# Performance work log

Measured on AMD Instinct MI355X. Metric: run time of the kernel, lower is better.

The kernel has to match this reference:

```python
import jax, jax.numpy as jnp
import numpy as np

INPUT_DIM = 3
OUTPUT_DIM = 3
HIDDEN = 128


def _lstm_layer(x, W_ih, W_hh, b_ih, b_hh):
    # x: (B, T, D_in); W_ih: (4H, D_in); W_hh: (4H, H); biases: (4H,)
    B, T, _ = x.shape
    H = W_hh.shape[1]
    # precompute input contribution for all timesteps (one big GEMM)
    xg = jnp.einsum('bti,gi->btg', x, W_ih) + b_ih + b_hh  # (B, T, 4H)
    h0 = jnp.zeros((B, H), dtype=x.dtype)
    c0 = jnp.zeros((B, H), dtype=x.dtype)

    def step(carry, xt):
        h, c = carry
        g = xt + h @ W_hh.T  # (B, 4H)
        i, f, gg, o = jnp.split(g, 4, axis=-1)  # PyTorch gate order: i, f, g, o
        i = jax.nn.sigmoid(i)
        f = jax.nn.sigmoid(f)
        gg = jnp.tanh(gg)
        o = jax.nn.sigmoid(o)
        c = f * c + i * gg
        h = o * jnp.tanh(c)
        return (h, c), h

    _, hs = jax.lax.scan(step, (h0, c0), jnp.swapaxes(xg, 0, 1))  # hs: (T, B, H)
    return jnp.swapaxes(hs, 0, 1)  # (B, T, H)


def setup_inputs() -> dict:
    key = jax.random.key(0)
    ks = jax.random.split(key, 11)
    B, T = 256, 1000
    s_in = 1.0 / np.sqrt(HIDDEN)
    inp = {
        'x': jax.random.normal(ks[0], (B, T, INPUT_DIM), dtype=jnp.float32),
        'W_ih_l0': jax.random.uniform(ks[1], (4 * HIDDEN, INPUT_DIM), jnp.float32, -s_in, s_in),
        'W_hh_l0': jax.random.uniform(ks[2], (4 * HIDDEN, HIDDEN), jnp.float32, -s_in, s_in),
        'b_ih_l0': jax.random.uniform(ks[3], (4 * HIDDEN,), jnp.float32, -s_in, s_in),
        'b_hh_l0': jax.random.uniform(ks[4], (4 * HIDDEN,), jnp.float32, -s_in, s_in),
        'W_ih_l1': jax.random.uniform(ks[5], (4 * HIDDEN, HIDDEN), jnp.float32, -s_in, s_in),
        'W_hh_l1': jax.random.uniform(ks[6], (4 * HIDDEN, HIDDEN), jnp.float32, -s_in, s_in),
        'b_ih_l1': jax.random.uniform(ks[7], (4 * HIDDEN,), jnp.float32, -s_in, s_in),
        'b_hh_l1': jax.random.uniform(ks[8], (4 * HIDDEN,), jnp.float32, -s_in, s_in),
        'fc_w': jax.random.uniform(ks[9], (OUTPUT_DIM, HIDDEN), jnp.float32, -s_in, s_in),
        'fc_b': jax.random.uniform(ks[10], (OUTPUT_DIM,), jnp.float32, -s_in, s_in),
    }
    return inp


def reference(x, W_ih_l0, W_hh_l0, b_ih_l0, b_hh_l0,
              W_ih_l1, W_hh_l1, b_ih_l1, b_hh_l1, fc_w, fc_b):
    # 2-layer LSTM (eval mode: inter-layer dropout is identity) + linear head
    h1 = _lstm_layer(x, W_ih_l0, W_hh_l0, b_ih_l0, b_hh_l0)
    h2 = _lstm_layer(h1, W_ih_l1, W_hh_l1, b_ih_l1, b_hh_l1)
    y = jnp.einsum('bth,oh->bto', h2, fc_w) + fc_b  # (B, T, OUTPUT_DIM)
    return y
```

## Files before the change

kernel.cpp:

```cpp
#include <hip/hip_runtime.h>

#define NB 256
#define TT 1000
#define HD 128
#define NG 512

#define WGA __attribute__((amdgpu_flat_work_group_size(512,512), amdgpu_waves_per_eu(2,2)))

typedef __attribute__((ext_vector_type(8))) short s8v;
typedef __attribute__((ext_vector_type(4))) float f4v;

__device__ __forceinline__ unsigned short bf16rne(float v) {
    unsigned u = __float_as_uint(v);
    unsigned r = u + 0x7FFF + ((u >> 16) & 1);
    return (unsigned short)(r >> 16);
}
__device__ __forceinline__ float bf16tof(unsigned short h) {
    return __uint_as_float(((unsigned)h) << 16);
}
__device__ __forceinline__ float sigf(float x) { return 1.f / (1.f + __expf(-x)); }
__device__ __forceinline__ float tanhfast(float x) {
    float e = __expf(-2.f * x);
    return 2.f / (1.f + e) - 1.f;
}

#define PKFMA(acc, h, w) \
    asm("v_pk_fma_f32 %0, %1, %2, %0" : "+v"(acc) : "v"(h), "v"(w))

__device__ __forceinline__ float2 lo2(float4 v) { return make_float2(v.x, v.y); }
__device__ __forceinline__ float2 hi2(float4 v) { return make_float2(v.z, v.w); }

#define DOT128P(h4, wv, P0, P1, P2, P3)                                        \
    {                                                                          \
        _Pragma("unroll")                                                      \
        for (int g = 0; g < 8; ++g) {                                          \
            float4 c0=(h4)[4*g+0], c1=(h4)[4*g+1],                             \
                   c2=(h4)[4*g+2], c3=(h4)[4*g+3];                             \
            PKFMA(P0, lo2(c0), lo2(wv[4*g+0]));                                \
            PKFMA(P1, hi2(c0), hi2(wv[4*g+0]));                                \
            PKFMA(P2, lo2(c1), lo2(wv[4*g+1]));                                \
            PKFMA(P3, hi2(c1), hi2(wv[4*g+1]));                                \
            PKFMA(P0, lo2(c2), lo2(wv[4*g+2]));                                \
            PKFMA(P1, hi2(c2), hi2(wv[4*g+2]));                                \
            PKFMA(P2, lo2(c3), lo2(wv[4*g+3]));                                \
            PKFMA(P3, hi2(c3), hi2(wv[4*g+3]));                                \
            __builtin_amdgcn_sched_barrier(0);                                 \
        }                                                                      \
    }

__global__ WGA
void lstm_layer0(const float* __restrict__ x,
                 const float* __restrict__ Wih, const float* __restrict__ Whh,
                 const float* __restrict__ bih, const float* __restrict__ bhh,
                 float* __restrict__ h1c,
                 float* __restrict__ hstate, float* __restrict__ cstate,
                 int t0, int len)
{
    __shared__ __align__(16) float h_lds[HD];
    __shared__ float gbuf[NG];
    __shared__ float x_lds[3 * TT];
    const int j = threadIdx.x;
    const int b = blockIdx.x;

    float4 wv[HD/4];
    {
        const float4* wr = (const float4*)(Whh + (size_t)j * HD);
        #pragma unroll
        for (int q = 0; q < HD/4; ++q) wv[q] = wr[q];
    }
    const float wx0 = Wih[j*3+0], wx1 = Wih[j*3+1], wx2 = Wih[j*3+2];
    const float bias = bih[j] + bhh[j];

    for (int idx = j; idx < 3*len; idx += 512)
        x_lds[idx] = x[((size_t)b*TT + t0)*3 + idx];

    float c = 0.f, hcur = 0.f;
    if (j < HD) {
        if (t0 != 0) { hcur = hstate[b*HD+j]; c = cstate[b*HD+j]; }
        h_lds[j] = hcur;
    }
    __syncthreads();

    const int gtype = j >> 7;
    for (int tc = 0; tc < len; ++tc) {
        float2 p0 = {0.f,0.f}, p1 = {0.f,0.f}, p2 = {0.f,0.f}, p3 = {0.f,0.f};
        const float4* h4 = (const float4*)h_lds;
        DOT128P(h4, wv, p0, p1, p2, p3);
        float acc = bias + ((p0.x+p0.y)+(p1.x+p1.y)) + ((p2.x+p2.y)+(p3.x+p3.y));
        acc = fmaf(wx0, x_lds[3*tc+0], acc);
        acc = fmaf(wx1, x_lds[3*tc+1], acc);
        acc = fmaf(wx2, x_lds[3*tc+2], acc);
        float act = (gtype == 2) ? tanhfast(acc) : sigf(acc);
        gbuf[j] = act;
        __syncthreads();
        if (j < HD) {
            float ig = gbuf[j], fg = gbuf[HD+j], gg = gbuf[2*HD+j], og = gbuf[3*HD+j];
            c = fmaf(fg, c, ig*gg);
            hcur = og * tanhfast(c);
            h_lds[j] = hcur;
            h1c[((size_t)b*len + tc)*HD + j] = hcur;
        }
        __syncthreads();
    }
    if (j < HD) { hstate[b*HD+j] = hcur; cstate[b*HD+j] = c; }
}

__global__ WGA
void xgate_gemm(const float* __restrict__ h1c,
                const float* __restrict__ Wih1,
                const float* __restrict__ bih1, const float* __restrict__ bhh1,
                float* __restrict__ xg1c, int len)
{
    __shared__ float bsum[NG];
    const int j = threadIdx.x;
    const int b = blockIdx.x;
    const int wv = j >> 6, lane = j & 63, lq = lane >> 4, lm = lane & 15;

    s8v Ah[4][4], Al[4][4];
    {
        #pragma unroll
        for (int t = 0; t < 4; ++t) {
            const int m = 64*wv + 16*t + lm;
            const float* wrow = Wih1 + (size_t)m * HD;
            #pragma unroll
            for (int kc = 0; kc < 4; ++kc) {
                const int k0 = 32*kc + 4*lq;
                float4 va = *(const float4*)(wrow + k0);
                float4 vb = *(const float4*)(wrow + k0 + 16);
                float vs[8] = {va.x,va.y,va.z,va.w,vb.x,vb.y,vb.z,vb.w};
                s8v ah, al;
                #pragma unroll
                for (int e = 0; e < 8; ++e) {
                    unsigned short hb = bf16rne(vs[e]);
                    float lo = vs[e] - bf16tof(hb);
                    ah[e] = (short)hb; al[e] = (short)bf16rne(lo);
                }
                Ah[t][kc] = ah; Al[t][kc] = al;
            }
        }
    }
    bsum[j] = bih1[j] + bhh1[j];
    __syncthreads();

    for (int ts = 0; ts < len; ts += 16) {
        const int trow = (ts + lm < len) ? (ts + lm) : (len - 1);
        const float* hrow = h1c + ((size_t)b*len + trow)*HD;
        s8v Bh[4], Bl[4];
        #pragma unroll
        for (int kc = 0; kc < 4; ++kc) {
            const int k0 = 32*kc + 4*lq;
            float4 va = *(const float4*)(hrow + k0);
            float4 vb = *(const float4*)(hrow + k0 + 16);
            float vs[8] = {va.x,va.y,va.z,va.w,vb.x,vb.y,vb.z,vb.w};
            s8v hh, hl;
            #pragma unroll
            for (int e = 0; e < 8; ++e) {
                unsigned short hb = bf16rne(vs[e]);
                float lo = vs[e] - bf16tof(hb);
                hh[e] = (short)hb; hl[e] = (short)bf16rne(lo);
            }
            Bh[kc] = hh; Bl[kc] = hl;
        }
        f4v zz = {0.f,0.f,0.f,0.f};
        f4v accA[4] = {zz,zz,zz,zz}, accB[4] = {zz,zz,zz,zz};
        #pragma unroll
        for (int kc = 0; kc < 4; ++kc) {
            #pragma unroll
            for (int t = 0; t < 4; ++t)
                accA[t] = __builtin_amdgcn_mfma_f32_16x16x32_bf16(Ah[t][kc], Bh[kc], accA[t], 0,0,0);
        }
        #pragma unroll
        for (int kc = 0; kc < 4; ++kc) {
            #pragma unroll
            for (int t = 0; t < 4; ++t)
                accB[t] = __builtin_amdgcn_mfma_f32_16x16x32_bf16(Al[t][kc], Bh[kc], accB[t], 0,0,0);
        }
        #pragma unroll
        for (int kc = 0; kc < 4; ++kc) {
            #pragma unroll
            for (int t = 0; t < 4; ++t)
                accB[t] = __builtin_amdgcn_mfma_f32_16x16x32_bf16(Ah[t][kc], Bl[kc], accB[t], 0,0,0);
        }
        if (ts + lm < len) {
            float* xrow = xg1c + ((size_t)b*len + ts + lm)*NG;
            #pragma unroll
            for (int t = 0; t < 4; ++t) {
                const int r0 = 64*wv + 16*t + 4*lq;
                float4 o;
                o.x = accA[t][0]+accB[t][0] + bsum[r0+0];
                o.y = accA[t][1]+accB[t][1] + bsum[r0+1];
                o.z = accA[t][2]+accB[t][2] + bsum[r0+2];
                o.w = accA[t][3]+accB[t][3] + bsum[r0+3];
                *(float4*)&xrow[r0] = o;
            }
        }
    }
}

__global__ WGA
void lstm_layer1(const float* __restrict__ xg1c,
                 const float* __restrict__ Whh1,
                 float* __restrict__ h2c,
                 float* __restrict__ hstate, float* __restrict__ cstate,
                 int t0, int len)
{
    __shared__ __align__(16) float h_lds[HD];
    __shared__ float gbuf[NG];
    const int j = threadIdx.x;
    const int b = blockIdx.x;
    float4 wv[HD/4];
    {
        const float4* wr = (const float4*)(Whh1 + (size_t)j * HD);
        #pragma unroll
        for (int q = 0; q < HD/4; ++q) wv[q] = wr[q];
    }
    float c = 0.f, hcur = 0.f;
    if (j < HD) {
        if (t0 != 0) { hcur = hstate[b*HD+j]; c = cstate[b*HD+j]; }
        h_lds[j] = hcur;
    }
    __syncthreads();
    const int gtype = j >> 7;
    float xg_cur = xg1c[((size_t)b*len + 0)*NG + j];
    for (int tc = 0; tc < len; ++tc) {
        float xg_nxt = 0.f;
        if (tc+1 < len) xg_nxt = xg1c[((size_t)b*len + tc+1)*NG + j];
        float2 p0 = {0.f,0.f}, p1 = {0.f,0.f}, p2 = {0.f,0.f}, p3 = {0.f,0.f};
        const float4* h4 = (const float4*)h_lds;
        DOT128P(h4, wv, p0, p1, p2, p3);
        float acc = xg_cur + ((p0.x+p0.y)+(p1.x+p1.y)) + ((p2.x+p2.y)+(p3.x+p3.y));
        float act = (gtype == 2) ? tanhfast(acc) : sigf(acc);
        gbuf[j] = act;
        __syncthreads();
        if (j < HD) {
            float ig = gbuf[j], fg = gbuf[HD+j], gg = gbuf[2*HD+j], og = gbuf[3*HD+j];
            c = fmaf(fg, c, ig*gg);
            hcur = og * tanhfast(c);
            h_lds[j] = hcur;
            h2c[((size_t)b*len + tc)*HD + j] = hcur;
        }
        __syncthreads();
        xg_cur = xg_nxt;
    }
    if (j < HD) { hstate[b*HD+j] = hcur; cstate[b*HD+j] = c; }
}

__global__ __launch_bounds__(512, 1)
void fc_head(const float* __restrict__ h2c,
             const float* __restrict__ fcw, const float* __restrict__ fcb,
             float* __restrict__ y, int t0, int len)
{
    const int b = blockIdx.x;
    const int wid = threadIdx.x >> 6;
    const int lane = threadIdx.x & 63;
    const float f0a = fcw[0*HD+lane], f0b = fcw[0*HD+64+lane];
    const float f1a = fcw[1*HD+lane], f1b = fcw[1*HD+64+lane];
    const float f2a = fcw[2*HD+lane], f2b = fcw[2*HD+64+lane];
    const float fb = (lane < 3) ? fcb[lane] : 0.f;
    for (int tc = wid; tc < len; tc += 8) {
        const float* hp = h2c + ((size_t)b*len + tc)*HD;
        float ha = hp[lane], hb = hp[64+lane];
        float y0 = ha*f0a + hb*f0b;
        float y1 = ha*f1a + hb*f1b;
        float y2 = ha*f2a + hb*f2b;
        #pragma unroll
        for (int m = 1; m < 64; m <<= 1) {
            y0 += __shfl_xor(y0, m);
            y1 += __shfl_xor(y1, m);
            y2 += __shfl_xor(y2, m);
        }
        if (lane < 3) {
            float yv = (lane==0) ? y0 : (lane==1) ? y1 : y2;
            y[((size_t)b*TT + (t0+tc))*3 + lane] = yv + fb;
        }
    }
}

extern "C" void kernel_launch(void* const* d_in, const int* in_sizes, int n_in,
                              void* d_out, int out_size, void* d_ws, size_t ws_size,
                              hipStream_t stream)
{
    const float* x    = (const float*)d_in[0];
    const float* Wih0 = (const float*)d_in[1];
    const float* Whh0 = (const float*)d_in[2];
    const float* bih0 = (const float*)d_in[3];
    const float* bhh0 = (const float*)d_in[4];
    const float* Wih1 = (const float*)d_in[5];
    const float* Whh1 = (const float*)d_in[6];
    const float* bih1 = (const float*)d_in[7];
    const float* bhh1 = (const float*)d_in[8];
    const float* fcw  = (const float*)d_in[9];
    const float* fcb  = (const float*)d_in[10];
    float* y = (float*)d_out;

    const size_t stateBytes = 4ull * NB * HD * sizeof(float);
    const size_t perT = (size_t)NB*HD*sizeof(float) + (size_t)NB*NG*sizeof(float);
    long tcl = (ws_size > stateBytes) ? (long)((ws_size - stateBytes) / perT) : 1;
    if (tcl > TT) tcl = TT;
    if (tcl < 1)  tcl = 1;
    const int Tc = (int)tcl;

    float* h1c  = (float*)d_ws;
    float* xg1c = h1c  + (size_t)NB * Tc * HD;
    float* hs1  = xg1c + (size_t)NB * Tc * NG;
    float* cs1  = hs1 + NB*HD;
    float* hs2  = cs1 + NB*HD;
    float* cs2  = hs2 + NB*HD;
    float* h2c  = h1c;

    for (int t0 = 0; t0 < TT; t0 += Tc) {
        const int len = (TT - t0 < Tc) ? (TT - t0) : Tc;
        lstm_layer0<<<dim3(NB), dim3(512), 0, stream>>>(
            x, Wih0, Whh0, bih0, bhh0, h1c, hs1, cs1, t0, len);
        xgate_gemm<<<dim3(NB), dim3(512), 0, stream>>>(
            h1c, Wih1, bih1, bhh1, xg1c, len);
        lstm_layer1<<<dim3(NB), dim3(512), 0, stream>>>(
            xg1c, Whh1, h2c, hs2, cs2, t0, len);
        fc_head<<<dim3(NB), dim3(512), 0, stream>>>(
            h2c, fcw, fcb, y, t0, len);
    }
}
```

Baseline: 1.952 ms.

## Remap gate rows per wavefront, combine gates via shuffles, double-buffer hidden state

Both recurrent LSTM kernels now assign each wavefront the four gate rows (i, f, g, o) of 16 hidden units, so the cell update can gather the gate activations with intra-wave shuffles instead of an LDS gate buffer. The hidden-state array is double-buffered, which removes one of the two block-wide barriers per timestep. Sigmoid and tanh are merged into a single branch-free exp-based formula with per-lane constants, avoiding divergent activation code. In exchange, only 16 of 64 lanes per wave do the cell update and global store, and the h stores become narrower per wave.

Result: faster. 1.893 ms (median of 2 runs) (-3.0%).

```diff
diff --git a/kernel.cpp b/kernel.cpp
--- a/kernel.cpp
+++ b/kernel.cpp
@@ -56,53 +56,64 @@
                  float* __restrict__ hstate, float* __restrict__ cstate,
                  int t0, int len)
 {
-    __shared__ __align__(16) float h_lds[HD];
-    __shared__ float gbuf[NG];
+    __shared__ __align__(16) float h_lds[2][HD];
     __shared__ float x_lds[3 * TT];
     const int j = threadIdx.x;
     const int b = blockIdx.x;
+    const int w  = j >> 6;
+    const int l  = j & 63;
+    const int g  = l >> 4;
+    const int jj = l & 15;
+    const int r  = g*HD + 16*w + jj;
+    const int hh = 16*w + jj;
 
     float4 wv[HD/4];
     {
-        const float4* wr = (const float4*)(Whh + (size_t)j * HD);
+        const float4* wr = (const float4*)(Whh + (size_t)r * HD);
         #pragma unroll
         for (int q = 0; q < HD/4; ++q) wv[q] = wr[q];
     }
-    const float wx0 = Wih[j*3+0], wx1 = Wih[j*3+1], wx2 = Wih[j*3+2];
-    const float bias = bih[j] + bhh[j];
+    const float wx0 = Wih[r*3+0], wx1 = Wih[r*3+1], wx2 = Wih[r*3+2];
+    const float bias = bih[r] + bhh[r];
+    const float am = (g == 2) ? -2.f : -1.f;
+    const float as = (g == 2) ?  2.f :  1.f;
+    const float at = (g == 2) ? -1.f :  0.f;
 
     for (int idx = j; idx < 3*len; idx += 512)
         x_lds[idx] = x[((size_t)b*TT + t0)*3 + idx];
 
     float c = 0.f, hcur = 0.f;
-    if (j < HD) {
-        if (t0 != 0) { hcur = hstate[b*HD+j]; c = cstate[b*HD+j]; }
-        h_lds[j] = hcur;
+    if (l < 16) {
+        if (t0 != 0) { hcur = hstate[b*HD+hh]; c = cstate[b*HD+hh]; }
+        h_lds[0][hh] = hcur;
     }
     __syncthreads();
 
-    const int gtype = j >> 7;
+    int cur = 0;
     for (int tc = 0; tc < len; ++tc) {
-        float2 p0 = {0.f,0.f}, p1 = {0.f,0.f}, p2 = {0.f,0.f}, p3 = {0.f,0.f};
-        const float4* h4 = (const float4*)h_lds;
+        float2 p0={0.f,0.f}, p1={0.f,0.f}, p2={0.f,0.f}, p3={0.f,0.f};
+        const float4* h4 = (const float4*)h_lds[cur];
         DOT128P(h4, wv, p0, p1, p2, p3);
         float acc = bias + ((p0.x+p0.y)+(p1.x+p1.y)) + ((p2.x+p2.y)+(p3.x+p3.y));
         acc = fmaf(wx0, x_lds[3*tc+0], acc);
         acc = fmaf(wx1, x_lds[3*tc+1], acc);
         acc = fmaf(wx2, x_lds[3*tc+2], acc);
-        float act = (gtype == 2) ? tanhfast(acc) : sigf(acc);
-        gbuf[j] = act;
+        float e = __expf(am * acc);
+        float act = as / (1.f + e) + at;
+        float iv = __shfl(act, jj);
+        float fv = __shfl(act, jj+16);
+        float gv = __shfl(act, jj+32);
+        float ov = __shfl(act, jj+48);
+        if (l < 16) {
+            c = fmaf(fv, c, iv*gv);
+            hcur = ov * tanhfast(c);
+            h_lds[cur^1][hh] = hcur;
+            h1c[((size_t)b*len + tc)*HD + hh] = hcur;
+        }
         __syncthreads();
-        if (j < HD) {
-            float ig = gbuf[j], fg = gbuf[HD+j], gg = gbuf[2*HD+j], og = gbuf[3*HD+j];
-            c = fmaf(fg, c, ig*gg);
-            hcur = og * tanhfast(c);
-            h_lds[j] = hcur;
-            h1c[((size_t)b*len + tc)*HD + j] = hcur;
-        }
-        __syncthreads();
-    }
-    if (j < HD) { hstate[b*HD+j] = hcur; cstate[b*HD+j] = c; }
+        cur ^= 1;
+    }
+    if (l < 16) { hstate[b*HD+hh] = hcur; cstate[b*HD+hh] = c; }
 }
 
 __global__ WGA
@@ -152,14 +163,14 @@
             float4 va = *(const float4*)(hrow + k0);
             float4 vb = *(const float4*)(hrow + k0 + 16);
             float vs[8] = {va.x,va.y,va.z,va.w,vb.x,vb.y,vb.z,vb.w};
-            s8v hh, hl;
+            s8v hhv, hlv;
             #pragma unroll
             for (int e = 0; e < 8; ++e) {
                 unsigned short hb = bf16rne(vs[e]);
                 float lo = vs[e] - bf16tof(hb);
-                hh[e] = (short)hb; hl[e] = (short)bf16rne(lo);
+                hhv[e] = (short)hb; hlv[e] = (short)bf16rne(lo);
             }
-            Bh[kc] = hh; Bl[kc] = hl;
+            Bh[kc] = hhv; Bl[kc] = hlv;
         }
         f4v zz = {0.f,0.f,0.f,0.f};
         f4v accA[4] = {zz,zz,zz,zz}, accB[4] = {zz,zz,zz,zz};
@@ -204,45 +215,59 @@
                  float* __restrict__ hstate, float* __restrict__ cstate,
                  int t0, int len)
 {
-    __shared__ __align__(16) float h_lds[HD];
-    __shared__ float gbuf[NG];
+    __shared__ __align__(16) float h_lds[2][HD];
     const int j = threadIdx.x;
     const int b = blockIdx.x;
+    const int w  = j >> 6;
+    const int l  = j & 63;
+    const int g  = l >> 4;
+    const int jj = l & 15;
+    const int r  = g*HD + 16*w + jj;
+    const int hh = 16*w + jj;
+
     float4 wv[HD/4];
     {
-        const float4* wr = (const float4*)(Whh1 + (size_t)j * HD);
+        const float4* wr = (const float4*)(Whh1 + (size_t)r * HD);
         #pragma unroll
         for (int q = 0; q < HD/4; ++q) wv[q] = wr[q];
     }
+    const float am = (g == 2) ? -2.f : -1.f;
+    const float as = (g == 2) ?  2.f :  1.f;
+    const float at = (g == 2) ? -1.f :  0.f;
+
     float c = 0.f, hcur = 0.f;
-    if (j < HD) {
-        if (t0 != 0) { hcur = hstate[b*HD+j]; c = cstate[b*HD+j]; }
-        h_lds[j] = hcur;
+    if (l < 16) {
+        if (t0 != 0) { hcur = hstate[b*HD+hh]; c = cstate[b*HD+hh]; }
+        h_lds[0][hh] = hcur;
     }
     __syncthreads();
-    const int gtype = j >> 7;
-    float xg_cur = xg1c[((size_t)b*len + 0)*NG + j];
+
+    float xg_cur = xg1c[((size_t)b*len + 0)*NG + r];
+    int cur = 0;
     for (int tc = 0; tc < len; ++tc) {
         float xg_nxt = 0.f;
-        if (tc+1 < len) xg_nxt = xg1c[((size_t)b*len + tc+1)*NG + j];
-        float2 p0 = {0.f,0.f}, p1 = {0.f,0.f}, p2 = {0.f,0.f}, p3 = {0.f,0.f};
-        const float4* h4 = (const float4*)h_lds;
+        if (tc+1 < len) xg_nxt = xg1c[((size_t)b*len + tc+1)*NG + r];
+        float2 p0={0.f,0.f}, p1={0.f,0.f}, p2={0.f,0.f}, p3={0.f,0.f};
+        const float4* h4 = (const float4*)h_lds[cur];
         DOT128P(h4, wv, p0, p1, p2, p3);
         float acc = xg_cur + ((p0.x+p0.y)+(p1.x+p1.y)) + ((p2.x+p2.y)+(p3.x+p3.y));
-        float act = (gtype == 2) ? tanhfast(acc) : sigf(acc);
-        gbuf[j] = act;
+        float e = __expf(am * acc);
+        float act = as / (1.f + e) + at;
+        float iv = __shfl(act, jj);
+        float fv = __shfl(act, jj+16);
+        float gv = __shfl(act, jj+32);
+        float ov = __shfl(act, jj+48);
+        if (l < 16) {
+            c = fmaf(fv, c, iv*gv);
+            hcur = ov * tanhfast(c);
+            h_lds[cur^1][hh] = hcur;
+            h2c[((size_t)b*len + tc)*HD + hh] = hcur;
+        }
         __syncthreads();
-        if (j < HD) {
-            float ig = gbuf[j], fg = gbuf[HD+j], gg = gbuf[2*HD+j], og = gbuf[3*HD+j];
-            c = fmaf(fg, c, ig*gg);
-            hcur = og * tanhfast(c);
-            h_lds[j] = hcur;
-            h2c[((size_t)b*len + tc)*HD + j] = hcur;
-        }
-        __syncthreads();
+        cur ^= 1;
         xg_cur = xg_nxt;
     }
-    if (j < HD) { hstate[b*HD+j] = hcur; cstate[b*HD+j] = c; }
+    if (l < 16) { hstate[b*HD+hh] = hcur; cstate[b*HD+hh] = c; }
 }
 
 __global__ __launch_bounds__(512, 1)
```
